# Performance work log

Hardware: AMD Instinct MI355X
Metric: run time of the kernel (lower is better)

Reference implementation:

```python
import math
import numpy as np
import jax
import jax.numpy as jnp

# ---- static representation structure (matches init_kwargs) ----
MUL = 16
RS = [(MUL, 0), (MUL, 1)]  # (multiplicity, l), parity 0 => all l_filters allowed
N_DIM = sum(m * (2 * l + 1) for m, l in RS)  # 64

def _lf(l_in, l_out):
    # o3.selection_rule: |l_in - l_out| .. l_in + l_out (parity 0 keeps all)
    return list(range(abs(l_in - l_out), l_in + l_out + 1))

SET_L = sorted({l for _, lo in RS for _, li in RS for l in _lf(li, lo)})  # [0,1,2]
Y_OFF = {}
_off = 0
for _l in SET_L:
    Y_OFF[_l] = _off
    _off += 2 * _l + 1
N_PATH = sum(mo * mi * len(_lf(li, lo)) for mo, lo in RS for mi, li in RS)  # 1536
RADIAL_H = 64

# ---- Clebsch-Gordan (real Wigner 3j) tables, computed once in numpy ----
def _f(n):
    return math.factorial(round(n))

def _su2_cg(j1, m1, j2, m2, j3, m3):
    if m3 != m1 + m2:
        return 0.0
    vmin = max(-j1 + j2 + m3, -j1 + m1, 0)
    vmax = min(j2 + j3 + m1, j3 - j1 + j2, j3 + m3)
    c = ((2 * j3 + 1) * _f(j3 + j1 - j2) * _f(j3 - j1 + j2) * _f(j1 + j2 - j3) / _f(j1 + j2 + j3 + 1)) ** 0.5 \
        * (_f(j3 + m3) * _f(j3 - m3) / (_f(j1 + m1) * _f(j1 - m1) * _f(j2 + m2) * _f(j2 - m2))) ** 0.5
    s = 0.0
    for v in range(vmin, vmax + 1):
        s += (-1.0) ** (v + j2 + m2) * _f(j2 + j3 + m1 - v) * _f(j1 - m1 + v) / (
            _f(v) * _f(j3 - j1 + j2 - v) * _f(j3 + m3 - v) * _f(v + j1 - j2 - m3))
    return c * s

def _w3j(l1, l2, l3):
    w = np.zeros((2 * l1 + 1, 2 * l2 + 1, 2 * l3 + 1))
    for m1 in range(-l1, l1 + 1):
        for m2 in range(-l2, l2 + 1):
            m3 = -(m1 + m2)
            if abs(m3) > l3:
                continue
            w[m1 + l1, m2 + l2, m3 + l3] = (-1.0) ** (l1 - l2 + m1 + m2) / (2 * l3 + 1) ** 0.5 \
                * _su2_cg(l1, m1, l2, m2, l3, -m3)
    return w

def _Q(l):
    # complex->real spherical-harmonics change of basis, rows = real m
    q = np.zeros((2 * l + 1, 2 * l + 1), dtype=complex)
    q[l, l] = 1.0
    s2 = 2.0 ** -0.5
    for m in range(1, l + 1):
        q[l + m, l - m] = s2
        q[l + m, l + m] = (-1) ** m * s2
        q[l - m, l - m] = 1j * s2
        q[l - m, l + m] = -1j * (-1) ** m * s2
    return q

def _real3j(l1, l2, l3):
    C = np.einsum('ai,bj,ck,ijk->abc', _Q(l1), _Q(l2), _Q(l3), _w3j(l1, l2, l3).astype(complex))
    k = int(np.argmax(np.abs(C)))
    ph = C.flat[k]
    if abs(ph) < 1e-12:
        return np.real(C)
    return np.real(C / (ph / abs(ph)))

CG = {}
for _mo, _lo in RS:
    for _mi, _li in RS:
        for _lfil in _lf(_li, _lo):
            if (_lo, _li, _lfil) not in CG:
                CG[(_lo, _li, _lfil)] = jnp.asarray(_real3j(_lo, _li, _lfil), jnp.float32)

# ---- norm_coef (normalization='norm'), as in __init__ ----
NORM = np.zeros((len(RS), len(RS), 2))
for _i, (_mo, _lo) in enumerate(RS):
    _nse = sum(mi * len(_lf(li, _lo)) for mi, li in RS)
    for _j, (_mi, _li) in enumerate(RS):
        _lm = math.sqrt(2 * _li + 1) * math.sqrt(4 * math.pi)
        NORM[_i, _j, 0] = _lm / math.sqrt(_nse)
        NORM[_i, _j, 1] = _lm / math.sqrt(_mi)
NORM_J = jnp.asarray(NORM, jnp.float32)

def _sh(r):
    # real spherical harmonics l=0,1,2 (m = -l..l), stacked -> [9, batch, A, B]
    x, y, z = r[..., 0], r[..., 1], r[..., 2]
    r2 = x * x + y * y + z * z
    inv = jax.lax.rsqrt(r2)
    inv2 = 1.0 / r2
    PI = math.pi
    c0 = 0.5 / math.sqrt(PI)
    c1 = math.sqrt(3.0 / (4 * PI))
    c2 = math.sqrt(15.0 / (4 * PI))
    c20 = math.sqrt(5.0 / (16 * PI))
    return jnp.stack([
        jnp.full_like(x, c0),
        c1 * y * inv, c1 * z * inv, c1 * x * inv,
        c2 * x * y * inv2, c2 * y * z * inv2, c20 * (3 * z * z - r2) * inv2,
        c2 * x * z * inv2, 0.5 * c2 * (x * x - y * y) * inv2,
    ], axis=0)

def _forward(r, W1, b1, W2, b2):
    batch, A, B, _ = r.shape
    radii = jnp.sqrt(jnp.sum(r * r, axis=-1))          # [batch, A, B]
    Y = _sh(r)                                         # [9, batch, A, B]
    h = jax.nn.silu(radii.reshape(-1, 1) @ W1 + b1)    # radial MLP
    R = (h @ W2 + b2).reshape(batch, A, B, N_PATH)
    nc = NORM_J[:, :, (radii == 0).astype(jnp.int32)]  # [2, 2, batch, A, B]
    kernel = jnp.zeros((batch, A, B, N_DIM, N_DIM), r.dtype)
    begin_R = 0
    begin_out = 0
    for i, (mo, lo) in enumerate(RS):
        d_out = mo * (2 * lo + 1)
        so = begin_out
        begin_out += d_out
        begin_in = 0
        for j, (mi, li) in enumerate(RS):
            d_in = mi * (2 * li + 1)
            si = begin_in
            begin_in += d_in
            lfs = _lf(li, lo)
            n = mo * mi * len(lfs)
            sub_R = R[..., begin_R:begin_R + n].reshape(batch, A, B, mo, mi, len(lfs))
            begin_R += n
            snc = nc[i, j]
            K = jnp.zeros((batch, A, B, mo, 2 * lo + 1, mi, 2 * li + 1), r.dtype)
            for k, lfil in enumerate(lfs):
                o = Y_OFF[lfil]
                K = K + jnp.einsum('ijk,kzab,zabuv,zab->zabuivj',
                                   CG[(lo, li, lfil)], Y[o:o + 2 * lfil + 1], sub_R[..., k], snc)
            kernel = kernel.at[..., so:so + d_out, si:si + d_in].set(K.reshape(batch, A, B, d_out, d_in))
    return kernel

def setup_inputs() -> dict:
    key = jax.random.key(0)
    k1, k2, k3 = jax.random.split(key, 3)
    r = jax.random.normal(k1, (16, 32, 32, 3), dtype=jnp.float32)
    W1 = jax.random.normal(k2, (1, RADIAL_H), dtype=jnp.float32)
    b1 = jnp.zeros((RADIAL_H,), jnp.float32)
    W2 = jax.random.normal(k3, (RADIAL_H, N_PATH), dtype=jnp.float32) / math.sqrt(RADIAL_H)
    b2 = jnp.zeros((N_PATH,), jnp.float32)
    return {"r": r, "W1": W1, "b1": b1, "W2": W2, "b2": b2}

def reference(r, W1, b1, W2, b2):
    return _forward(r, W1, b1, W2, b2)
```

## Files before the change

kernel.cpp:

```cpp
#include <hip/hip_runtime.h>
#include <stdint.h>


#define PPW   16
#define NPATH 1536
#define HSTR  68
#define RSTR  1552
#define CSTR  36

__device__ __forceinline__ unsigned short f2bf(float f) {
    union { float f; uint32_t u; } v; v.f = f;
    return (unsigned short)((v.u + 0x7FFFu + ((v.u >> 16) & 1u)) >> 16);
}
__device__ __forceinline__ float bf2f(unsigned short s) {
    union { float f; uint32_t u; } v; v.u = ((uint32_t)s) << 16;
    return v.f;
}

__global__ __launch_bounds__(256, 2)
void qm9_fused(const float* __restrict__ rin, const float* __restrict__ W1,
               const float* __restrict__ b1, const float* __restrict__ W2,
               const float* __restrict__ b2, float* __restrict__ out)
{
    __shared__ float          h_lds[PPW][HSTR];
    __shared__ unsigned short R_lds[PPW][RSTR];
    __shared__ float          coef[PPW][CSTR];

    const int t  = threadIdx.x;
    const int wg = blockIdx.x;
    const int p  = t >> 4;
    const int g  = t & 15;
    const int pt = wg * PPW + p;

    {
        const float x = rin[3*pt+0], y = rin[3*pt+1], z = rin[3*pt+2];
        const float r2  = x*x + y*y + z*z;
        const float rad = sqrtf(r2);
        #pragma unroll
        for (int d = 0; d < 4; ++d) {
            const int k = 4*g + d;
            const float pre = rad * W1[k] + b1[k];
            h_lds[p][k] = pre / (1.0f + expf(-pre));
        }
    }
    if (t < PPW) {
        const int pp = wg * PPW + t;
        const float x = rin[3*pp+0], y = rin[3*pp+1], z = rin[3*pp+2];
        const float r2   = x*x + y*y + z*z;
        const float inv  = rsqrtf(r2);
        const float inv2 = 1.0f / r2;
        const float c0  = 0.28209479177387814f;
        const float c1  = 0.48860251190291992f;
        const float c2  = 1.09254843059207907f;
        const float c20 = 0.31539156525252005f;
        const float Y1 = c1*y*inv, Y2 = c1*z*inv, Y3 = c1*x*inv;
        const float Y4 = c2*x*y*inv2, Y5 = c2*y*z*inv2;
        const float Y6 = c20*(3.0f*z*z - r2)*inv2;
        const float Y7 = c2*x*z*inv2;
        const float Y8 = 0.5f*c2*(x*x - y*y)*inv2;
        const bool z0 = (r2 == 0.0f);
        const float n00 = z0 ? 0.88622692545275801f : 0.62665706865775012f;
        const float n01 = z0 ? 1.53499006295944860f : 1.08540188766074740f;
        const float n10 = z0 ? 0.88622692545275801f : 0.44311346272637900f;
        const float n11 = z0 ? 1.53499006295944860f : 0.76749503147972430f;
        const float SQ3I  = 0.57735026918962584f;
        const float SQ6I  = 0.40824829046386302f;
        const float SQ10I = 0.31622776601683794f;
        const float SQ30I = 0.18257418583505536f;
        float* cf = &coef[t][0];
        cf[0] = c0 * n00;
        cf[1] = SQ3I * n01 * Y1;
        cf[2] = SQ3I * n01 * Y2;
        cf[3] = SQ3I * n01 * Y3;
        cf[4] = SQ3I * n10 * Y1;
        cf[5] = SQ3I * n10 * Y2;
        cf[6] = SQ3I * n10 * Y3;
        const float d0 = SQ3I * c0 * n11;
        const float e  = SQ6I * n11;
        cf[7+ 0]=d0;   cf[7+ 1]=0.0f;    cf[7+ 2]=n11*(-SQ30I*Y6 - SQ10I*Y8);
        cf[7+ 3]=0.0f; cf[7+ 4]= e*Y3;   cf[7+ 5]=n11*( SQ10I*Y5);
        cf[7+ 6]=0.0f; cf[7+ 7]=-e*Y2;   cf[7+ 8]=n11*( SQ10I*Y4);
        cf[7+ 9]=0.0f; cf[7+10]=-e*Y3;   cf[7+11]=n11*( SQ10I*Y5);
        cf[7+12]=d0;   cf[7+13]=0.0f;    cf[7+14]=n11*( 2.0f*SQ30I*Y6);
        cf[7+15]=0.0f; cf[7+16]= e*Y1;   cf[7+17]=n11*( SQ10I*Y7);
        cf[7+18]=0.0f; cf[7+19]= e*Y2;   cf[7+20]=n11*( SQ10I*Y4);
        cf[7+21]=0.0f; cf[7+22]=-e*Y1;   cf[7+23]=n11*( SQ10I*Y7);
        cf[7+24]=d0;   cf[7+25]=0.0f;    cf[7+26]=n11*(-SQ30I*Y6 + SQ10I*Y8);
    }
    __syncthreads();

    {
        float acc[6][16];
        #pragma unroll
        for (int c = 0; c < 6; ++c) {
            const float bb = b2[t + 256*c];
            #pragma unroll
            for (int q = 0; q < 16; ++q) acc[c][q] = bb;
        }
        for (int k0 = 0; k0 < 64; k0 += 4) {
            float hk[16][4];
            #pragma unroll
            for (int q = 0; q < 16; ++q) {
                const float4 hv = *(const float4*)&h_lds[q][k0];
                hk[q][0]=hv.x; hk[q][1]=hv.y; hk[q][2]=hv.z; hk[q][3]=hv.w;
            }
            float w[4][6];
            #pragma unroll
            for (int d = 0; d < 4; ++d) {
                const float* wr = W2 + (size_t)(k0+d)*NPATH + t;
                #pragma unroll
                for (int c = 0; c < 6; ++c) w[d][c] = wr[256*c];
            }
            #pragma unroll
            for (int c = 0; c < 6; ++c) {
                #pragma unroll
                for (int q = 0; q < 16; ++q) {
                    float s = acc[c][q];
                    #pragma unroll
                    for (int d = 0; d < 4; ++d) s += hk[q][d] * w[d][c];
                    acc[c][q] = s;
                }
            }
        }
        #pragma unroll
        for (int c = 0; c < 6; ++c)
            #pragma unroll
            for (int q = 0; q < 16; ++q)
                R_lds[q][t + 256*c] = f2bf(acc[c][q]);
    }
    __syncthreads();

    {
        const float* cf = &coef[p][0];
        const float s00 = cf[0];
        const float bI[3] = {cf[4], cf[5], cf[6]};
        int vq[4], jq[4], mq[4];
        float aj[4];
        const int cc0 = 4*g - 16;
        const int v0  = (g >= 4) ? (cc0 / 3) : 0;
        #pragma unroll
        for (int d = 0; d < 4; ++d) {
            const int cc = (g >= 4) ? (cc0 + d) : 0;
            vq[d] = cc / 3;
            jq[d] = cc - 3*vq[d];
            mq[d] = (vq[d] != v0);
            aj[d] = cf[1 + jq[d]];
        }
        float Wd[4][3][3];
        if (g >= 4) {
            #pragma unroll
            for (int d = 0; d < 4; ++d)
                #pragma unroll
                for (int i = 0; i < 3; ++i)
                    #pragma unroll
                    for (int l = 0; l < 3; ++l)
                        Wd[d][i][l] = cf[7 + (i*3 + jq[d])*3 + l];
        }
        const unsigned short* Rp = &R_lds[p][0];
        float* outp = out + (size_t)pt * 4096 + 4*g;

        for (int u = 0; u < 16; ++u) {
            float v[4];
            if (g < 4) {
                const ushort4 rv = *(const ushort4*)&Rp[u*16 + 4*g];
                v[0]=s00*bf2f(rv.x); v[1]=s00*bf2f(rv.y);
                v[2]=s00*bf2f(rv.z); v[3]=s00*bf2f(rv.w);
            } else {
                #pragma unroll
                for (int d = 0; d < 4; ++d)
                    v[d] = aj[d] * bf2f(Rp[256 + u*16 + vq[d]]);
            }
            *(float4*)(outp + (size_t)u*64) = make_float4(v[0],v[1],v[2],v[3]);
        }
        for (int u = 0; u < 16; ++u) {
            float rA[4];
            float rsel[4][3];
            if (g < 4) {
                const ushort4 rv = *(const ushort4*)&Rp[512 + u*16 + 4*g];
                rA[0]=bf2f(rv.x); rA[1]=bf2f(rv.y); rA[2]=bf2f(rv.z); rA[3]=bf2f(rv.w);
            } else {
                float rB[2][3];
                const int base = 768 + (u*16 + v0)*3;
                #pragma unroll
                for (int w2 = 0; w2 < 2; ++w2)
                    #pragma unroll
                    for (int l = 0; l < 3; ++l)
                        rB[w2][l] = bf2f(Rp[base + 3*w2 + l]);
                #pragma unroll
                for (int d = 0; d < 4; ++d)
                    #pragma unroll
                    for (int l = 0; l < 3; ++l)
                        rsel[d][l] = mq[d] ? rB[1][l] : rB[0][l];
            }
            #pragma unroll
            for (int i = 0; i < 3; ++i) {
                float v[4];
                if (g < 4) {
                    #pragma unroll
                    for (int d = 0; d < 4; ++d) v[d] = bI[i] * rA[d];
                } else {
                    #pragma unroll
                    for (int d = 0; d < 4; ++d)
                        v[d] = Wd[d][i][0]*rsel[d][0] + Wd[d][i][1]*rsel[d][1]
                             + Wd[d][i][2]*rsel[d][2];
                }
                *(float4*)(outp + (size_t)(16 + 3*u + i)*64) = make_float4(v[0],v[1],v[2],v[3]);
            }
        }
    }
}

extern "C" void kernel_launch(void* const* d_in, const int* in_sizes, int n_in,
                              void* d_out, int out_size, void* d_ws, size_t ws_size,
                              hipStream_t stream) {
    const float* r  = (const float*)d_in[0];
    const float* W1 = (const float*)d_in[1];
    const float* b1 = (const float*)d_in[2];
    const float* W2 = (const float*)d_in[3];
    const float* b2 = (const float*)d_in[4];
    float* out = (float*)d_out;
    qm9_fused<<<dim3(1024), dim3(256), 0, stream>>>(r, W1, b1, W2, b2, out);
}
```

Measured before the change: 292.9 us.

## Compute radial MLP second layer with bf16 MFMA using pre-transposed W2

```diff
diff --git a/kernel.cpp b/kernel.cpp
--- a/kernel.cpp
+++ b/kernel.cpp
@@ -4,9 +4,11 @@
 
 #define PPW   16
 #define NPATH 1536
-#define HSTR  68
-#define RSTR  1552
-#define CSTR  36
+#define RSTR  1540
+#define CSTR  34
+
+typedef __attribute__((ext_vector_type(8))) short short8;
+typedef __attribute__((ext_vector_type(4))) float float4v;
 
 __device__ __forceinline__ unsigned short f2bf(float f) {
     union { float f; uint32_t u; } v; v.f = f;
@@ -17,12 +19,19 @@
     return v.f;
 }
 
-__global__ __launch_bounds__(256, 2)
+__global__ void w2_prep(const float* __restrict__ W2, unsigned short* __restrict__ W2T) {
+    const int idx = blockIdx.x * 256 + threadIdx.x;
+    if (idx < 64 * NPATH) {
+        const int n = idx >> 6, k = idx & 63;
+        W2T[idx] = f2bf(W2[(size_t)k * NPATH + n]);
+    }
+}
+
+__global__ __launch_bounds__(256, 3)
 void qm9_fused(const float* __restrict__ rin, const float* __restrict__ W1,
-               const float* __restrict__ b1, const float* __restrict__ W2,
+               const float* __restrict__ b1, const unsigned short* __restrict__ W2T,
                const float* __restrict__ b2, float* __restrict__ out)
 {
-    __shared__ float          h_lds[PPW][HSTR];
     __shared__ unsigned short R_lds[PPW][RSTR];
     __shared__ float          coef[PPW][CSTR];
 
@@ -31,18 +40,35 @@
     const int p  = t >> 4;
     const int g  = t & 15;
     const int pt = wg * PPW + p;
-
+    const int wave = t >> 6;
+    const int m  = t & 15;
+    const int q  = (t >> 4) & 3;
+
+    short8 afrag[2];
     {
-        const float x = rin[3*pt+0], y = rin[3*pt+1], z = rin[3*pt+2];
-        const float r2  = x*x + y*y + z*z;
-        const float rad = sqrtf(r2);
+        const int ptm = wg * PPW + m;
+        const float x = rin[3*ptm+0], y = rin[3*ptm+1], z = rin[3*ptm+2];
+        const float rad = sqrtf(x*x + y*y + z*z);
         #pragma unroll
-        for (int d = 0; d < 4; ++d) {
-            const int k = 4*g + d;
-            const float pre = rad * W1[k] + b1[k];
-            h_lds[p][k] = pre / (1.0f + expf(-pre));
-        }
-    }
+        for (int kb = 0; kb < 2; ++kb) {
+            const int k0 = kb*32 + q*8;
+            const float4 w1a = *(const float4*)&W1[k0];
+            const float4 w1b = *(const float4*)&W1[k0+4];
+            const float4 b1a = *(const float4*)&b1[k0];
+            const float4 b1b = *(const float4*)&b1[k0+4];
+            float pre[8];
+            pre[0]=rad*w1a.x+b1a.x; pre[1]=rad*w1a.y+b1a.y;
+            pre[2]=rad*w1a.z+b1a.z; pre[3]=rad*w1a.w+b1a.w;
+            pre[4]=rad*w1b.x+b1b.x; pre[5]=rad*w1b.y+b1b.y;
+            pre[6]=rad*w1b.z+b1b.z; pre[7]=rad*w1b.w+b1b.w;
+            #pragma unroll
+            for (int j = 0; j < 8; ++j) {
+                const float hv = pre[j] / (1.0f + expf(-pre[j]));
+                afrag[kb][j] = (short)f2bf(hv);
+            }
+        }
+    }
+
     if (t < PPW) {
         const int pp = wg * PPW + t;
         const float x = rin[3*pp+0], y = rin[3*pp+1], z = rin[3*pp+2];
@@ -87,46 +113,21 @@
         cf[7+21]=0.0f; cf[7+22]=-e*Y1;   cf[7+23]=n11*( SQ10I*Y7);
         cf[7+24]=d0;   cf[7+25]=0.0f;    cf[7+26]=n11*(-SQ30I*Y6 + SQ10I*Y8);
     }
-    __syncthreads();
 
     {
-        float acc[6][16];
-        #pragma unroll
-        for (int c = 0; c < 6; ++c) {
-            const float bb = b2[t + 256*c];
-            #pragma unroll
-            for (int q = 0; q < 16; ++q) acc[c][q] = bb;
-        }
-        for (int k0 = 0; k0 < 64; k0 += 4) {
-            float hk[16][4];
-            #pragma unroll
-            for (int q = 0; q < 16; ++q) {
-                const float4 hv = *(const float4*)&h_lds[q][k0];
-                hk[q][0]=hv.x; hk[q][1]=hv.y; hk[q][2]=hv.z; hk[q][3]=hv.w;
-            }
-            float w[4][6];
-            #pragma unroll
-            for (int d = 0; d < 4; ++d) {
-                const float* wr = W2 + (size_t)(k0+d)*NPATH + t;
-                #pragma unroll
-                for (int c = 0; c < 6; ++c) w[d][c] = wr[256*c];
-            }
-            #pragma unroll
-            for (int c = 0; c < 6; ++c) {
-                #pragma unroll
-                for (int q = 0; q < 16; ++q) {
-                    float s = acc[c][q];
-                    #pragma unroll
-                    for (int d = 0; d < 4; ++d) s += hk[q][d] * w[d][c];
-                    acc[c][q] = s;
-                }
-            }
-        }
-        #pragma unroll
-        for (int c = 0; c < 6; ++c)
-            #pragma unroll
-            for (int q = 0; q < 16; ++q)
-                R_lds[q][t + 256*c] = f2bf(acc[c][q]);
+        for (int i = wave; i < 96; i += 4) {
+            const int n0  = i * 16;
+            const int col = n0 + m;
+            const short8 b0 = *(const short8*)(W2T + (size_t)col*64 + q*8);
+            const short8 b1f = *(const short8*)(W2T + (size_t)col*64 + 32 + q*8);
+            float4v acc = {0.0f, 0.0f, 0.0f, 0.0f};
+            acc = __builtin_amdgcn_mfma_f32_16x16x32_bf16(afrag[0], b0,  acc, 0, 0, 0);
+            acc = __builtin_amdgcn_mfma_f32_16x16x32_bf16(afrag[1], b1f, acc, 0, 0, 0);
+            const float bias = b2[col];
+            #pragma unroll
+            for (int r = 0; r < 4; ++r)
+                R_lds[q*4 + r][col] = f2bf(acc[r] + bias);
+        }
     }
     __syncthreads();
 
@@ -219,5 +220,8 @@
     const float* W2 = (const float*)d_in[3];
     const float* b2 = (const float*)d_in[4];
     float* out = (float*)d_out;
-    qm9_fused<<<dim3(1024), dim3(256), 0, stream>>>(r, W1, b1, W2, b2, out);
-}
+    unsigned short* W2T = (unsigned short*)d_ws;
+
+    w2_prep<<<dim3((64*NPATH + 255)/256), dim3(256), 0, stream>>>(W2, W2T);
+    qm9_fused<<<dim3(1024), dim3(256), 0, stream>>>(r, W1, b1, W2T, b2, out);
+}
```

After: 283.5 us. 1.03x faster.
